# Kernel tuning notes

Measured on AMD Instinct MI355X. Metric: run time of the kernel, lower is better.

The kernel has to match this reference:

```python
import jax, jax.numpy as jnp
import numpy as np

B, S, D, F, E = 8, 2048, 1024, 4096, 5

def setup_inputs() -> dict:
    key = jax.random.key(0)
    ks = jax.random.split(key, 9)
    sc = 0.02
    return {
        "hidden_states": jax.random.normal(ks[0], (B, S, D), jnp.float32),
        "type_label": jax.random.randint(ks[1], (B,), 0, E, jnp.int32),
        "wi": jax.random.normal(ks[2], (E, D, F), jnp.float32) * sc,   # routed experts wi
        "wo": jax.random.normal(ks[3], (E, F, D), jnp.float32) * sc,   # routed experts wo
        "swi": jax.random.normal(ks[4], (2, D, F), jnp.float32) * sc,  # shared experts wi
        "swo": jax.random.normal(ks[5], (2, F, D), jnp.float32) * sc,  # shared experts wo
        "g1": jax.random.normal(ks[6], (3 * D, D), jnp.float32) * sc,  # gate layer 1
        "g2": jax.random.normal(ks[7], (D, 3), jnp.float32) * sc,      # gate layer 2
    }

def _dense(x, wi_, wo_):
    # T5DenseActDense with relu act, dropout=0 (eval)
    return jax.nn.relu(x @ wi_) @ wo_

def reference(hidden_states, type_label, wi, wo, swi, swo, g1, g2):
    x = hidden_states
    s0 = _dense(x, swi[0], swo[0])  # [B,S,D] shared expert 0
    s1 = _dense(x, swi[1], swo[1])  # [B,S,D] shared expert 1
    # per-sample routed expert: gather weights by label, batched GEMM
    wi_sel = wi[type_label]         # [B,D,F]
    wo_sel = wo[type_label]         # [B,F,D]
    h = jax.nn.relu(jnp.einsum('bsd,bdf->bsf', x, wi_sel))
    eo = jnp.einsum('bsf,bfd->bsd', h, wo_sel)  # [B,S,D]
    # gate on token 0 of each stream, all gates share parameters
    gate_in = jnp.concatenate([eo[:, 0], s0[:, 0], s1[:, 0]], axis=-1)  # [B,3D]
    w = jax.nn.softmax(jax.nn.relu(gate_in @ g1) @ g2, axis=-1)         # [B,3]
    w = w[:, :, None, None]
    return eo * w[:, 0] + s0 * w[:, 1] + s1 * w[:, 2]
```

## Files before the change

### kernel.cpp

```cpp
#include <hip/hip_runtime.h>
#include <hip/hip_bf16.h>
#include <cstdint>

#define B_ 8
#define S_ 2048
#define D_ 1024
#define F_ 4096
#define E_ 5

typedef __attribute__((ext_vector_type(4))) int      i32x4;
typedef __attribute__((ext_vector_type(4))) float    f32x4;
typedef __attribute__((ext_vector_type(4))) uint16_t u16x4;
typedef __attribute__((ext_vector_type(8))) uint16_t u16x8;

__device__ __forceinline__ float b2f(uint16_t u){
  union { uint32_t i; float f; } v; v.i = ((uint32_t)u) << 16; return v.f;
}
__device__ __forceinline__ uint16_t f2b(float f){
  union { float f; uint32_t i; } v; v.f = f;
  uint32_t x = v.i;
  uint32_t r = (x + 0x7FFFu + ((x >> 16) & 1u)) >> 16;
  return (uint16_t)r;
}
__device__ __forceinline__ void gload16B(const uint16_t* g, uint16_t* l){
  __builtin_amdgcn_global_load_lds(
      (const __attribute__((address_space(1))) void*)g,
      (__attribute__((address_space(3))) void*)l, 16, 0, 0);
}

__global__ __launch_bounds__(256) void cvt_bf16(
    const float* __restrict__ src, uint16_t* __restrict__ dst, long n)
{
  long i = ((long)blockIdx.x * 256 + threadIdx.x) * 8;
  const long stride = (long)gridDim.x * 256 * 8;
  for (; i + 8 <= n; i += stride){
    f32x4 a = *(const f32x4*)(src + i);
    f32x4 b = *(const f32x4*)(src + i + 4);
    u16x8 r;
#pragma unroll
    for (int k = 0; k < 4; ++k){ r[k] = f2b(a[k]); r[4 + k] = f2b(b[k]); }
    *(u16x8*)(dst + i) = r;
  }
}

__global__ __launch_bounds__(256) void transpose64(
    const float* __restrict__ src, uint16_t* __restrict__ dst, int R, int C)
{
  __shared__ uint16_t t[64][68];
  const size_t base = (size_t)blockIdx.z * R * C;
  const int r0 = blockIdx.x * 64, c0 = blockIdx.y * 64;
  const int tr = threadIdx.x >> 4;
  const int tc = (threadIdx.x & 15) * 4;
#pragma unroll
  for (int i = 0; i < 4; ++i){
    const int row = tr + i * 16;
    f32x4 v = *(const f32x4*)(src + base + (size_t)(r0 + row) * C + (c0 + tc));
    t[row][tc + 0] = f2b(v[0]); t[row][tc + 1] = f2b(v[1]);
    t[row][tc + 2] = f2b(v[2]); t[row][tc + 3] = f2b(v[3]);
  }
  __syncthreads();
#pragma unroll
  for (int i = 0; i < 4; ++i){
    const int orow = tr + i * 16;
    u16x4 v;
    v[0] = t[tc + 0][orow]; v[1] = t[tc + 1][orow];
    v[2] = t[tc + 2][orow]; v[3] = t[tc + 3][orow];
    *(u16x4*)(dst + base + (size_t)(c0 + orow) * R + (r0 + tc)) = v;
  }
}

__global__ __launch_bounds__(256) void transpose_f32(
    const float* __restrict__ src, float* __restrict__ dst, int R, int C)
{
  __shared__ float t[64][65];
  const int r0 = blockIdx.x * 64, c0 = blockIdx.y * 64;
  const int tr = threadIdx.x >> 4;
  const int tc = (threadIdx.x & 15) * 4;
#pragma unroll
  for (int i = 0; i < 4; ++i){
    const int row = tr + i * 16;
    f32x4 v = *(const f32x4*)(src + (size_t)(r0 + row) * C + (c0 + tc));
    t[row][tc + 0] = v[0]; t[row][tc + 1] = v[1];
    t[row][tc + 2] = v[2]; t[row][tc + 3] = v[3];
  }
  __syncthreads();
#pragma unroll
  for (int i = 0; i < 4; ++i){
    const int orow = tr + i * 16;
    f32x4 v;
    v[0] = t[tc + 0][orow]; v[1] = t[tc + 1][orow];
    v[2] = t[tc + 2][orow]; v[3] = t[tc + 3][orow];
    *(f32x4*)(dst + (size_t)(c0 + orow) * R + (r0 + tc)) = v;
  }
}

__global__ __launch_bounds__(256) void gate_h(
    const uint16_t* __restrict__ xb, const uint16_t* __restrict__ wiT,
    const uint16_t* __restrict__ swiT, const int* __restrict__ label,
    float* __restrict__ hbuf)
{
  const int wv = threadIdx.x >> 6, lane = threadIdx.x & 63;
  const int f = blockIdx.x * 4 + wv;
  const int path = blockIdx.y, b = blockIdx.z;
  const uint16_t* wrow = (path == 0)
      ? wiT  + ((size_t)label[b] * F_ + f) * D_
      : swiT + ((size_t)(path - 1) * F_ + f) * D_;
  const uint16_t* xr = xb + (size_t)b * S_ * D_;
  float acc = 0.f;
#pragma unroll
  for (int c = 0; c < 2; ++c){
    const int off = c * 512 + lane * 8;
    u16x8 w  = *(const u16x8*)(wrow + off);
    u16x8 xv = *(const u16x8*)(xr + off);
#pragma unroll
    for (int k = 0; k < 8; ++k) acc += b2f(xv[k]) * b2f(w[k]);
  }
#pragma unroll
  for (int o = 32; o > 0; o >>= 1) acc += __shfl_down(acc, o);
  if (lane == 0)
    hbuf[(size_t)(b * 3 + path) * F_ + f] = fmaxf(acc, 0.f);
}

__global__ __launch_bounds__(256) void gate_row(
    const uint16_t* __restrict__ woT, const uint16_t* __restrict__ swoT,
    const int* __restrict__ label, const float* __restrict__ hbuf,
    float* __restrict__ gin)
{
  const int wv = threadIdx.x >> 6, lane = threadIdx.x & 63;
  const int d = blockIdx.x * 4 + wv;
  const int path = blockIdx.y, b = blockIdx.z;
  const uint16_t* wrow = (path == 0)
      ? woT  + ((size_t)label[b] * D_ + d) * F_
      : swoT + ((size_t)(path - 1) * D_ + d) * F_;
  const float* hb = hbuf + (size_t)(b * 3 + path) * F_;
  float acc = 0.f;
#pragma unroll
  for (int c = 0; c < 8; ++c){
    const int off = c * 512 + lane * 8;
    u16x8 w  = *(const u16x8*)(wrow + off);
    f32x4 h0 = *(const f32x4*)(hb + off);
    f32x4 h1 = *(const f32x4*)(hb + off + 4);
    acc += h0[0]*b2f(w[0]) + h0[1]*b2f(w[1]) + h0[2]*b2f(w[2]) + h0[3]*b2f(w[3])
         + h1[0]*b2f(w[4]) + h1[1]*b2f(w[5]) + h1[2]*b2f(w[6]) + h1[3]*b2f(w[7]);
  }
#pragma unroll
  for (int o = 32; o > 0; o >>= 1) acc += __shfl_down(acc, o);
  if (lane == 0)
    gin[(size_t)(b * 3 + path) * D_ + d] = acc;
}

__global__ __launch_bounds__(256) void gate_w1(
    const float* __restrict__ gin, const float* __restrict__ g1T,
    float* __restrict__ ts)
{
  const int wv = threadIdx.x >> 6, lane = threadIdx.x & 63;
  const int j = blockIdx.x * 4 + wv;
  const int b = blockIdx.y;
  const float* grow = g1T + (size_t)j * (3 * D_);
  const float* g = gin + (size_t)b * 3 * D_;
  float acc = 0.f;
#pragma unroll
  for (int c = 0; c < 12; ++c){
    const int off = c * 256 + lane * 4;
    f32x4 w  = *(const f32x4*)(grow + off);
    f32x4 gv = *(const f32x4*)(g + off);
    acc += gv[0]*w[0] + gv[1]*w[1] + gv[2]*w[2] + gv[3]*w[3];
  }
#pragma unroll
  for (int o = 32; o > 0; o >>= 1) acc += __shfl_down(acc, o);
  if (lane == 0)
    ts[(size_t)b * D_ + j] = fmaxf(acc, 0.f);
}

__global__ __launch_bounds__(256) void gate_w2(
    const float* __restrict__ ts, const float* __restrict__ g2,
    float* __restrict__ wgate)
{
  const int b = blockIdx.x;
  __shared__ float p0[256], p1[256], p2[256];
  const float* t = ts + (size_t)b * D_;
  float s0 = 0.f, s1 = 0.f, s2 = 0.f;
  const int j0 = threadIdx.x * 4;
#pragma unroll
  for (int jj = 0; jj < 4; ++jj){
    const float tv = t[j0 + jj];
    s0 += tv * g2[(j0 + jj) * 3 + 0];
    s1 += tv * g2[(j0 + jj) * 3 + 1];
    s2 += tv * g2[(j0 + jj) * 3 + 2];
  }
  p0[threadIdx.x] = s0; p1[threadIdx.x] = s1; p2[threadIdx.x] = s2;
  __syncthreads();
  for (int st = 128; st > 0; st >>= 1){
    if (threadIdx.x < st){
      p0[threadIdx.x] += p0[threadIdx.x + st];
      p1[threadIdx.x] += p1[threadIdx.x + st];
      p2[threadIdx.x] += p2[threadIdx.x + st];
    }
    __syncthreads();
  }
  if (threadIdx.x == 0){
    const float a = p0[0], c = p1[0], d = p2[0];
    const float m = fmaxf(a, fmaxf(c, d));
    const float e0 = expf(a - m), e1 = expf(c - m), e2 = expf(d - m);
    const float inv = 1.f / (e0 + e1 + e2);
    wgate[b * 3 + 0] = e0 * inv;
    wgate[b * 3 + 1] = e1 * inv;
    wgate[b * 3 + 2] = e2 * inv;
  }
}

template<int MODE>
__global__ __launch_bounds__(256, 4) void gemm_bt(
    const uint16_t* __restrict__ Abase, size_t a_stride, int lda, int K,
    const uint16_t* __restrict__ Wexp, const uint16_t* __restrict__ Wsh,
    int path, int b0, const int* __restrict__ label,
    const float* __restrict__ wgate,
    void* __restrict__ Obase_, size_t o_stride, int ldo)
{
  __shared__ uint16_t As[128 * 64];
  __shared__ uint16_t Bs[128 * 64];

  const int z  = blockIdx.z;
  const int b  = b0 + z;
  const int m0 = blockIdx.x * 128;
  const int n0 = blockIdx.y * 128;

  const uint16_t* A = Abase + (size_t)z * a_stride;
  const size_t wstride = (size_t)D_ * F_;
  const uint16_t* BT = (path == 0) ? Wexp + (size_t)label[b] * wstride
                                   : Wsh  + (size_t)(path - 1) * wstride;

  const int tid  = threadIdx.x;
  const int wave = tid >> 6;
  const int lane = tid & 63;

  const uint16_t* gA = A  + (size_t)(m0 + wave * 8 + (lane >> 3)) * lda + (lane & 7) * 8;
  const uint16_t* gB = BT + (size_t)(n0 + wave * 8 + (lane >> 3)) * K   + (lane & 7) * 8;
  uint16_t* lA = As + wave * 512;
  uint16_t* lB = Bs + wave * 512;

  f32x4 acc[4][4];
#pragma unroll
  for (int i = 0; i < 4; ++i)
#pragma unroll
    for (int j = 0; j < 4; ++j) acc[i][j] = (f32x4)0.0f;

  const uint16_t* pa = As + ((wave >> 1) * 64 + (lane & 15)) * 64 + (lane >> 4) * 8;
  const uint16_t* pb = Bs + ((wave &  1) * 64 + (lane & 15)) * 64 + (lane >> 4) * 8;

  const int KT = K >> 6;
  for (int kt = 0; kt < KT; ++kt){
    __syncthreads();
#pragma unroll
    for (int q = 0; q < 4; ++q){
      gload16B(gA + (size_t)q * 32 * lda, lA + q * 2048);
      gload16B(gB + (size_t)q * 32 * K,   lB + q * 2048);
    }
    gA += 64; gB += 64;
    __syncthreads();
#pragma unroll
    for (int ks = 0; ks < 2; ++ks){
      i32x4 af[4], bf[4];
#pragma unroll
      for (int i = 0; i < 4; ++i) af[i] = *(const i32x4*)(pa + i * 1024 + ks * 32);
#pragma unroll
      for (int j = 0; j < 4; ++j) bf[j] = *(const i32x4*)(pb + j * 1024 + ks * 32);
#pragma unroll
      for (int i = 0; i < 4; ++i)
#pragma unroll
        for (int j = 0; j < 4; ++j)
          asm("v_mfma_f32_16x16x32_bf16 %0, %1, %2, %0"
              : "+v"(acc[i][j]) : "v"(af[i]), "v"(bf[j]));
    }
  }

  asm volatile("s_nop 7\n\ts_nop 7" ::);

  const int orow0 = m0 + (wave >> 1) * 64 + (lane >> 4) * 4;
  const int ocol0 = n0 + (wave &  1) * 64 + (lane & 15);

  if constexpr (MODE == 0){
    uint16_t* O = (uint16_t*)Obase_ + (size_t)z * o_stride;
#pragma unroll
    for (int i = 0; i < 4; ++i)
#pragma unroll
      for (int j = 0; j < 4; ++j){
        const int col = ocol0 + j * 16;
#pragma unroll
        for (int r = 0; r < 4; ++r){
          const int row = orow0 + i * 16 + r;
          const float v = acc[i][j][r];
          O[(size_t)row * ldo + col] = f2b(v > 0.f ? v : 0.f);
        }
      }
  } else {
    float* O = (float*)Obase_ + (size_t)z * o_stride;
    const float scale = wgate[b * 3 + path];
#pragma unroll
    for (int i = 0; i < 4; ++i)
#pragma unroll
      for (int j = 0; j < 4; ++j){
        const int col = ocol0 + j * 16;
#pragma unroll
        for (int r = 0; r < 4; ++r){
          const int row = orow0 + i * 16 + r;
          const size_t idx = (size_t)row * ldo + col;
          float v = scale * acc[i][j][r];
          if constexpr (MODE == 2) v += O[idx];
          O[idx] = v;
        }
      }
  }
}

extern "C" void kernel_launch(void* const* d_in, const int* in_sizes, int n_in,
                              void* d_out, int out_size, void* d_ws, size_t ws_size,
                              hipStream_t stream)
{
  (void)in_sizes; (void)n_in; (void)out_size;
  const float* x    = (const float*)d_in[0];
  const int*   label= (const int*)d_in[1];
  const float* wi   = (const float*)d_in[2];
  const float* wo   = (const float*)d_in[3];
  const float* swi  = (const float*)d_in[4];
  const float* swo  = (const float*)d_in[5];
  const float* g1   = (const float*)d_in[6];
  const float* g2   = (const float*)d_in[7];
  float* out = (float*)d_out;

  char* ws = (char*)d_ws;
  float* wgate = (float*)ws;
  float* gin   = (float*)(ws + 256);
  float* hbuf  = (float*)(ws + 98560);
  float* ts    = (float*)(ws + 491776);
  float* g1T   = (float*)(ws + (1u << 20));
  uint16_t* xb = (uint16_t*)(ws + (16u << 20));
  size_t off = (size_t)(16u << 20) + (size_t)B_ * S_ * D_ * 2;
  uint16_t* wiT  = (uint16_t*)(ws + off); off += (size_t)E_ * D_ * F_ * 2;
  uint16_t* swiT = (uint16_t*)(ws + off); off += (size_t)2  * D_ * F_ * 2;
  uint16_t* woT  = (uint16_t*)(ws + off); off += (size_t)E_ * D_ * F_ * 2;
  uint16_t* swoT = (uint16_t*)(ws + off); off += (size_t)2  * D_ * F_ * 2;
  uint16_t* H    = (uint16_t*)(ws + off);
  const size_t hbytes = (size_t)S_ * F_ * 2;
  const size_t hcap = (ws_size > off) ? (ws_size - off) / hbytes : 0;
  const int nb = hcap >= 8 ? 8 : hcap >= 4 ? 4 : hcap >= 2 ? 2 : 1;

  cvt_bf16<<<dim3(2048), 256, 0, stream>>>(x, xb, (long)B_ * S_ * D_);
  transpose64<<<dim3(D_/64, F_/64, E_), 256, 0, stream>>>(wi,  wiT,  D_, F_);
  transpose64<<<dim3(D_/64, F_/64, 2 ), 256, 0, stream>>>(swi, swiT, D_, F_);
  transpose64<<<dim3(F_/64, D_/64, E_), 256, 0, stream>>>(wo,  woT,  F_, D_);
  transpose64<<<dim3(F_/64, D_/64, 2 ), 256, 0, stream>>>(swo, swoT, F_, D_);
  transpose_f32<<<dim3(3*D_/64, D_/64), 256, 0, stream>>>(g1, g1T, 3*D_, D_);

  gate_h  <<<dim3(F_/4, 3, B_), 256, 0, stream>>>(xb, wiT, swiT, label, hbuf);
  gate_row<<<dim3(D_/4, 3, B_), 256, 0, stream>>>(woT, swoT, label, hbuf, gin);
  gate_w1 <<<dim3(D_/4, B_),    256, 0, stream>>>(gin, g1T, ts);
  gate_w2 <<<dim3(B_),          256, 0, stream>>>(ts, g2, wgate);

  const size_t SD = (size_t)S_ * D_;
  const size_t SF = (size_t)S_ * F_;
  for (int path = 0; path < 3; ++path){
    for (int b0 = 0; b0 < B_; b0 += nb){
      const int nbc = (b0 + nb <= B_) ? nb : (B_ - b0);
      gemm_bt<0><<<dim3(S_/128, F_/128, nbc), 256, 0, stream>>>(
          xb + (size_t)b0 * SD, SD, D_, D_, wiT, swiT, path, b0, label,
          (const float*)nullptr, H, SF, F_);
      if (path == 0)
        gemm_bt<1><<<dim3(S_/128, D_/128, nbc), 256, 0, stream>>>(
            H, SF, F_, F_, woT, swoT, path, b0, label, wgate,
            out + (size_t)b0 * SD, SD, D_);
      else
        gemm_bt<2><<<dim3(S_/128, D_/128, nbc), 256, 0, stream>>>(
            H, SF, F_, F_, woT, swoT, path, b0, label, wgate,
            out + (size_t)b0 * SD, SD, D_);
    }
  }
}
```

Baseline: 1.130 ms.

## Double-buffer GEMM LDS tiles with async global-to-LDS prefetch of next K-slice

Splits the 64-wide K tile into two 32-wide LDS buffers and prefetches the next slice with global_load_lds while MFMAs run on the current one. Explicit vmcnt waits and raw barriers replace the two __syncthreads per iteration, and setprio is raised around the MFMA block. This aims to hide global memory latency behind compute, at the cost of twice as many loop iterations and barriers per K. LDS use stays the same.

```diff
diff --git a/kernel.cpp b/kernel.cpp
--- a/kernel.cpp
+++ b/kernel.cpp
@@ -27,6 +27,11 @@
       (const __attribute__((address_space(1))) void*)g,
       (__attribute__((address_space(3))) void*)l, 16, 0, 0);
 }
+
+#define FENCE  asm volatile("" ::: "memory")
+#define BARRIER { FENCE; __builtin_amdgcn_s_barrier(); FENCE; }
+#define LGKM0  asm volatile("s_waitcnt lgkmcnt(0)" ::: "memory")
+#define VMW(n) asm volatile("s_waitcnt vmcnt(" #n ")" ::: "memory")
 
 __global__ __launch_bounds__(256) void cvt_bf16(
     const float* __restrict__ src, uint16_t* __restrict__ dst, long n)
@@ -217,8 +222,8 @@
     const float* __restrict__ wgate,
     void* __restrict__ Obase_, size_t o_stride, int ldo)
 {
-  __shared__ uint16_t As[128 * 64];
-  __shared__ uint16_t Bs[128 * 64];
+  __shared__ uint16_t As[2][128 * 32];
+  __shared__ uint16_t Bs[2][128 * 32];
 
   const int z  = blockIdx.z;
   const int b  = b0 + z;
@@ -234,10 +239,8 @@
   const int wave = tid >> 6;
   const int lane = tid & 63;
 
-  const uint16_t* gA = A  + (size_t)(m0 + wave * 8 + (lane >> 3)) * lda + (lane & 7) * 8;
-  const uint16_t* gB = BT + (size_t)(n0 + wave * 8 + (lane >> 3)) * K   + (lane & 7) * 8;
-  uint16_t* lA = As + wave * 512;
-  uint16_t* lB = Bs + wave * 512;
+  const uint16_t* gA = A  + (size_t)(m0 + wave * 32 + (lane >> 2)) * lda + (lane & 3) * 8;
+  const uint16_t* gB = BT + (size_t)(n0 + wave * 32 + (lane >> 2)) * K   + (lane & 3) * 8;
 
   f32x4 acc[4][4];
 #pragma unroll
@@ -245,34 +248,54 @@
 #pragma unroll
     for (int j = 0; j < 4; ++j) acc[i][j] = (f32x4)0.0f;
 
-  const uint16_t* pa = As + ((wave >> 1) * 64 + (lane & 15)) * 64 + (lane >> 4) * 8;
-  const uint16_t* pb = Bs + ((wave &  1) * 64 + (lane & 15)) * 64 + (lane >> 4) * 8;
-
-  const int KT = K >> 6;
+  const int fa = ((wave >> 1) * 64 + (lane & 15)) * 32 + (lane >> 4) * 8;
+  const int fb = ((wave &  1) * 64 + (lane & 15)) * 32 + (lane >> 4) * 8;
+
+#define STAGE32(sel, kt) do {                                                \
+    const uint16_t* _ga = gA + (size_t)(kt) * 32;                            \
+    const uint16_t* _gb = gB + (size_t)(kt) * 32;                            \
+    _Pragma("unroll")                                                        \
+    for (int q = 0; q < 2; ++q){                                             \
+      gload16B(_ga + (size_t)q * 16 * lda, &As[sel][wave * 1024 + q * 512]); \
+      gload16B(_gb + (size_t)q * 16 * K,   &Bs[sel][wave * 1024 + q * 512]); \
+    }                                                                        \
+  } while (0)
+
+  const int KT = K >> 5;
+
+  STAGE32(0, 0);
+
   for (int kt = 0; kt < KT; ++kt){
-    __syncthreads();
-#pragma unroll
-    for (int q = 0; q < 4; ++q){
-      gload16B(gA + (size_t)q * 32 * lda, lA + q * 2048);
-      gload16B(gB + (size_t)q * 32 * K,   lB + q * 2048);
+    const int sel = kt & 1;
+    if (kt + 1 < KT){
+      STAGE32(sel ^ 1, kt + 1);
+      VMW(4);
+    } else {
+      VMW(0);
     }
-    gA += 64; gB += 64;
-    __syncthreads();
-#pragma unroll
-    for (int ks = 0; ks < 2; ++ks){
-      i32x4 af[4], bf[4];
-#pragma unroll
-      for (int i = 0; i < 4; ++i) af[i] = *(const i32x4*)(pa + i * 1024 + ks * 32);
-#pragma unroll
-      for (int j = 0; j < 4; ++j) bf[j] = *(const i32x4*)(pb + j * 1024 + ks * 32);
-#pragma unroll
-      for (int i = 0; i < 4; ++i)
-#pragma unroll
-        for (int j = 0; j < 4; ++j)
-          asm("v_mfma_f32_16x16x32_bf16 %0, %1, %2, %0"
-              : "+v"(acc[i][j]) : "v"(af[i]), "v"(bf[j]));
-    }
-  }
+    BARRIER;
+
+    const uint16_t* pa = &As[sel][fa];
+    const uint16_t* pb = &Bs[sel][fb];
+    i32x4 af[4], bf[4];
+#pragma unroll
+    for (int i = 0; i < 4; ++i) af[i] = *(const i32x4*)(pa + i * 512);
+#pragma unroll
+    for (int j = 0; j < 4; ++j) bf[j] = *(const i32x4*)(pb + j * 512);
+    __builtin_amdgcn_s_setprio(1);
+#pragma unroll
+    for (int i = 0; i < 4; ++i)
+#pragma unroll
+      for (int j = 0; j < 4; ++j)
+        asm("v_mfma_f32_16x16x32_bf16 %0, %1, %2, %0"
+            : "+v"(acc[i][j]) : "v"(af[i]), "v"(bf[j]));
+    __builtin_amdgcn_s_setprio(0);
+
+    __builtin_amdgcn_sched_barrier(0);
+    LGKM0;
+    BARRIER;
+  }
+#undef STAGE32
 
   asm volatile("s_nop 7\n\ts_nop 7" ::);
 
```

Measured after the change: 1.229 ms. 1.09x slower.
